# Kernel optimization log

Measured on AMD Instinct MI355X. Metric: run time of the kernel, lower is better.

## Reference

```python
import jax, jax.numpy as jnp
import numpy as np

N = 8388608

def setup_inputs() -> dict:
    key = jax.random.key(0)
    k1, k2 = jax.random.split(key)
    preds = jax.random.normal(k1, (N, 5), dtype=jnp.float32)
    target = jax.random.normal(k2, (N, 3), dtype=jnp.float32)
    return {"preds": preds, "target": target}

def reference(preds, target):
    # main MSE over the first 3 quantile columns: [N, 3]
    main_mse = (preds[:, :3] - target[:, :3]) ** 2

    p2 = preds[:, 2]
    p3 = preds[:, 3]
    t2 = target[:, 2]

    # lower-range loss, vectorized form of the per-row if/elif/else: [N]
    lower = jnp.where(
        p3 > p2,
        jnp.float32(1000.0),
        jnp.where(p3 > t2 * 0.95, jnp.float32(0.0), (p3 - t2 * 0.95) ** 2),
    )

    # NOTE: the original code assigns upper_range_loss = torch.Tensor(lowe_range_loss),
    # i.e. the upper range loss is (buggily) a copy of the lower range loss.
    # We replicate that behavior faithfully.
    upper = lower

    # concatenate all loss elements (3N + N + N) and reduce with mean
    loss = jnp.concatenate([main_mse.ravel(), lower, upper])
    return jnp.mean(loss)
```

## Files before the change

kernel.cpp:

```cpp
#include <hip/hip_runtime.h>


#define NROWS 8388608

__global__ void __launch_bounds__(256) qloss_partial(
    const float* __restrict__ preds,
    const float* __restrict__ target,
    double* __restrict__ ws)
{
    const int ngroups = NROWS / 4;
    const int tid = blockIdx.x * blockDim.x + threadIdx.x;
    const int stride = gridDim.x * blockDim.x;

    double acc = 0.0;

    for (int g = tid; g < ngroups; g += stride) {
        const float4* p4 = (const float4*)(preds + (size_t)g * 20);
        const float4* t4 = (const float4*)(target + (size_t)g * 12);

        float p[20];
        float t[12];
        *(float4*)(p + 0)  = p4[0];
        *(float4*)(p + 4)  = p4[1];
        *(float4*)(p + 8)  = p4[2];
        *(float4*)(p + 12) = p4[3];
        *(float4*)(p + 16) = p4[4];
        *(float4*)(t + 0)  = t4[0];
        *(float4*)(t + 4)  = t4[1];
        *(float4*)(t + 8)  = t4[2];

        float sum = 0.0f;
        #pragma unroll
        for (int r = 0; r < 4; ++r) {
            const float a0 = p[5*r + 0] - t[3*r + 0];
            const float a1 = p[5*r + 1] - t[3*r + 1];
            const float a2 = p[5*r + 2] - t[3*r + 2];
            const float m  = a0*a0 + a1*a1 + a2*a2;

            const float pp2 = p[5*r + 2];
            const float pp3 = p[5*r + 3];
            const float q   = t[3*r + 2] * 0.95f;
            const float d   = pp3 - q;
            const float lower = (pp3 > pp2) ? 1000.0f
                              : ((pp3 > q) ? 0.0f : d * d);
            sum += m + 2.0f * lower;
        }
        acc += (double)sum;
    }

    #pragma unroll
    for (int off = 32; off > 0; off >>= 1)
        acc += __shfl_down(acc, off, 64);

    __shared__ double lds[4];
    const int lane = threadIdx.x & 63;
    const int wave = threadIdx.x >> 6;
    if (lane == 0) lds[wave] = acc;
    __syncthreads();

    if (threadIdx.x == 0) {
        double s = lds[0] + lds[1] + lds[2] + lds[3];
        atomicAdd(ws, s);
    }
}

__global__ void qloss_final(const double* __restrict__ ws, float* __restrict__ out)
{
    *out = (float)(*ws / (5.0 * (double)NROWS));
}

extern "C" void kernel_launch(void* const* d_in, const int* in_sizes, int n_in,
                              void* d_out, int out_size, void* d_ws, size_t ws_size,
                              hipStream_t stream)
{
    const float* preds  = (const float*)d_in[0];
    const float* target = (const float*)d_in[1];
    float* out  = (float*)d_out;
    double* ws  = (double*)d_ws;

    hipMemsetAsync(ws, 0, sizeof(double), stream);

    qloss_partial<<<2048, 256, 0, stream>>>(preds, target, ws);
    qloss_final<<<1, 1, 0, stream>>>(ws, out);
}
```

Measured before the change: 296.5 us.

## Stage row chunks through LDS with coalesced float4 loads

Each block now loads a 1024-row chunk of preds and target with fully coalesced float4 loads into shared memory, then reads its rows back from LDS. This replaces per-thread strided 80-byte and 48-byte vector loads, which were poorly coalesced across a wavefront. The cost is an extra LDS write and read per element, two barriers per chunk, and 32KB of LDS per block.

```diff
diff --git a/kernel.cpp b/kernel.cpp
--- a/kernel.cpp
+++ b/kernel.cpp
@@ -2,65 +2,78 @@
 
 
 #define NROWS 8388608
+#define ROWS_PER_CHUNK 1024
+#define NCHUNKS (NROWS / ROWS_PER_CHUNK)
+#define PCHUNK (ROWS_PER_CHUNK * 5)
+#define TCHUNK (ROWS_PER_CHUNK * 3)
 
 __global__ void __launch_bounds__(256) qloss_partial(
     const float* __restrict__ preds,
     const float* __restrict__ target,
     double* __restrict__ ws)
 {
-    const int ngroups = NROWS / 4;
-    const int tid = blockIdx.x * blockDim.x + threadIdx.x;
-    const int stride = gridDim.x * blockDim.x;
+    __shared__ float sp[PCHUNK];
+    __shared__ float st[TCHUNK];
 
+    const int t = threadIdx.x;
     double acc = 0.0;
 
-    for (int g = tid; g < ngroups; g += stride) {
-        const float4* p4 = (const float4*)(preds + (size_t)g * 20);
-        const float4* t4 = (const float4*)(target + (size_t)g * 12);
+    for (int chunk = blockIdx.x; chunk < NCHUNKS; chunk += gridDim.x) {
+        const float4* gp = (const float4*)(preds + (size_t)chunk * PCHUNK);
+        const float4* gt = (const float4*)(target + (size_t)chunk * TCHUNK);
 
-        float p[20];
-        float t[12];
-        *(float4*)(p + 0)  = p4[0];
-        *(float4*)(p + 4)  = p4[1];
-        *(float4*)(p + 8)  = p4[2];
-        *(float4*)(p + 12) = p4[3];
-        *(float4*)(p + 16) = p4[4];
-        *(float4*)(t + 0)  = t4[0];
-        *(float4*)(t + 4)  = t4[1];
-        *(float4*)(t + 8)  = t4[2];
+        float4 rp[5], rt[3];
+        #pragma unroll
+        for (int k = 0; k < 5; ++k) rp[k] = gp[t + k * 256];
+        #pragma unroll
+        for (int k = 0; k < 3; ++k) rt[k] = gt[t + k * 256];
+        #pragma unroll
+        for (int k = 0; k < 5; ++k) ((float4*)sp)[t + k * 256] = rp[k];
+        #pragma unroll
+        for (int k = 0; k < 3; ++k) ((float4*)st)[t + k * 256] = rt[k];
+
+        __syncthreads();
 
         float sum = 0.0f;
         #pragma unroll
-        for (int r = 0; r < 4; ++r) {
-            const float a0 = p[5*r + 0] - t[3*r + 0];
-            const float a1 = p[5*r + 1] - t[3*r + 1];
-            const float a2 = p[5*r + 2] - t[3*r + 2];
+        for (int rr = 0; rr < 4; ++rr) {
+            const int r = t + rr * 256;
+            const float p0 = sp[5*r + 0];
+            const float p1 = sp[5*r + 1];
+            const float p2 = sp[5*r + 2];
+            const float p3 = sp[5*r + 3];
+            const float t0 = st[3*r + 0];
+            const float t1 = st[3*r + 1];
+            const float t2 = st[3*r + 2];
+
+            const float a0 = p0 - t0;
+            const float a1 = p1 - t1;
+            const float a2 = p2 - t2;
             const float m  = a0*a0 + a1*a1 + a2*a2;
 
-            const float pp2 = p[5*r + 2];
-            const float pp3 = p[5*r + 3];
-            const float q   = t[3*r + 2] * 0.95f;
-            const float d   = pp3 - q;
-            const float lower = (pp3 > pp2) ? 1000.0f
-                              : ((pp3 > q) ? 0.0f : d * d);
+            const float q = t2 * 0.95f;
+            const float d = p3 - q;
+            const float lower = (p3 > p2) ? 1000.0f : ((p3 > q) ? 0.0f : d * d);
+
             sum += m + 2.0f * lower;
         }
         acc += (double)sum;
+
+        __syncthreads();
     }
 
     #pragma unroll
     for (int off = 32; off > 0; off >>= 1)
         acc += __shfl_down(acc, off, 64);
 
-    __shared__ double lds[4];
-    const int lane = threadIdx.x & 63;
-    const int wave = threadIdx.x >> 6;
-    if (lane == 0) lds[wave] = acc;
+    __shared__ double red[4];
+    const int lane = t & 63;
+    const int wave = t >> 6;
+    if (lane == 0) red[wave] = acc;
     __syncthreads();
 
-    if (threadIdx.x == 0) {
-        double s = lds[0] + lds[1] + lds[2] + lds[3];
-        atomicAdd(ws, s);
+    if (t == 0) {
+        atomicAdd(ws, red[0] + red[1] + red[2] + red[3]);
     }
 }
 
```

After: 296.8 us. No clear change (+0.1%).
